# Kernel optimization log

Hardware: AMD Instinct MI355X
Metric: run time of the kernel (lower is better)

Reference implementation:

```python
import jax, jax.numpy as jnp
import numpy as np

SOS = 1

def setup_inputs() -> dict:
    key = jax.random.key(0)
    ks = jax.random.split(key, 12)
    B, S, T, H, V = 64, 128, 32, 1024, 32000
    sc = 0.02
    return {
        'encoder_outputs': jax.random.normal(ks[0], (B, S, H), jnp.float32),
        'encoder_hidden': jax.random.normal(ks[1], (1, B, H), jnp.float32),
        'target_tensor': jax.random.randint(ks[2], (B, T), 0, V),
        'embedding': jax.random.normal(ks[3], (V, H), jnp.float32) * sc,
        'Wa': jax.random.normal(ks[4], (H, H), jnp.float32) * sc,
        'ba': jnp.zeros((H,), jnp.float32),
        'Ua': jax.random.normal(ks[5], (H, H), jnp.float32) * sc,
        'bu': jnp.zeros((H,), jnp.float32),
        'Va': jax.random.normal(ks[6], (1, H), jnp.float32) * sc,
        'bv': jnp.zeros((1,), jnp.float32),
        'W_ih': jax.random.normal(ks[7], (3 * H, 2 * H), jnp.float32) * sc,
        'b_ih': jnp.zeros((3 * H,), jnp.float32),
        'W_hh': jax.random.normal(ks[8], (3 * H, H), jnp.float32) * sc,
        'b_hh': jnp.zeros((3 * H,), jnp.float32),
        'W_out': jax.random.normal(ks[9], (V, H), jnp.float32) * sc,
        'b_out': jnp.zeros((V,), jnp.float32),
    }

def reference(encoder_outputs, encoder_hidden, target_tensor, embedding,
              Wa, ba, Ua, bu, Va, bv, W_ih, b_ih, W_hh, b_hh, W_out, b_out):
    B, S, H = encoder_outputs.shape
    T = target_tensor.shape[1]
    # teacher forcing: input at step i is SOS for i=0 else target[:, i-1]
    tokens = jnp.concatenate([jnp.full((B, 1), SOS, target_tensor.dtype),
                              target_tensor[:, :-1]], axis=1)  # (B,T)
    emb = embedding[tokens]  # (B,T,H); dropout is identity (eval)
    keys_proj = jnp.einsum('bsh,gh->bsg', encoder_outputs, Ua) + bu  # Ua(keys), (B,S,H)
    h0 = encoder_hidden[0]  # (B,H)

    def step(h, x_t):
        # Bahdanau attention: Va(tanh(Wa q + Ua k))
        q = h @ Wa.T + ba  # (B,H)
        scores = jnp.einsum('bsh,h->bs', jnp.tanh(q[:, None, :] + keys_proj), Va[0]) + bv[0]
        w = jax.nn.softmax(scores, axis=-1)  # (B,S)
        ctx = jnp.einsum('bs,bsh->bh', w, encoder_outputs)
        x = jnp.concatenate([x_t, ctx], axis=-1)  # (B,2H)
        # GRU cell (PyTorch convention)
        gi = x @ W_ih.T + b_ih
        gh = h @ W_hh.T + b_hh
        ir, iz, inn = jnp.split(gi, 3, axis=-1)
        hr, hz, hn = jnp.split(gh, 3, axis=-1)
        r = jax.nn.sigmoid(ir + hr)
        z = jax.nn.sigmoid(iz + hz)
        n = jnp.tanh(inn + r * hn)
        h_new = (1.0 - z) * n + z * h
        logits = h_new @ W_out.T + b_out  # (B,V)
        return h_new, (logits, w)

    h_final, (logits, weights) = jax.lax.scan(step, h0, jnp.swapaxes(emb, 0, 1))
    log_probs = jax.nn.log_softmax(jnp.swapaxes(logits, 0, 1), axis=-1)  # (B,T,V)
    attentions = jnp.swapaxes(weights, 0, 1)  # (B,T,S)
    return log_probs, h_final[None], attentions
```

## Files before the change

kernel.cpp:

```cpp
#include <hip/hip_runtime.h>


typedef unsigned short u16;
typedef __bf16 bf16x8 __attribute__((ext_vector_type(8)));
typedef float f32x4 __attribute__((ext_vector_type(4)));
typedef u16 u16x8 __attribute__((ext_vector_type(8)));

#define DEV __device__ __forceinline__

DEV u16 f2b(float f) {
  union { float f; unsigned u; } v; v.f = f;
  unsigned r = v.u + 0x7fffu + ((v.u >> 16) & 1u);
  return (u16)(r >> 16);
}
DEV float b2f(u16 b) {
  union { unsigned u; float f; } v; v.u = ((unsigned)b) << 16;
  return v.f;
}
DEV float sigm(float x) { return 1.f / (1.f + __expf(-x)); }
DEV float ftanh(float x) {
  x = fminf(fmaxf(x, -20.f), 20.f);
  float e = __expf(2.f * x);
  return (e - 1.f) / (e + 1.f);
}
DEV void gl16(const void* g, void* l) {
  __builtin_amdgcn_global_load_lds((const __attribute__((address_space(1))) void*)g,
                                   (__attribute__((address_space(3))) void*)l, 16, 0, 0);
}

__global__ __launch_bounds__(256) void prepk(const float* __restrict__ enc, const float* __restrict__ Ua,
                                             const float* __restrict__ Wa, const float* __restrict__ Whh,
                                             const float* __restrict__ Wout, const float* __restrict__ Wih,
                                             const float* __restrict__ embd, const int* __restrict__ tgt,
                                             const float* __restrict__ eh, u16* __restrict__ enc_b,
                                             u16* __restrict__ Ua_b, u16* __restrict__ Wa_b,
                                             u16* __restrict__ Whh_b, u16* __restrict__ Wout_b,
                                             u16* __restrict__ Wih1_b, u16* __restrict__ Wih2_b,
                                             u16* __restrict__ emb_b, float* __restrict__ hf,
                                             u16* __restrict__ hb0) {
  const long q0 = 2097152;
  const long q1 = q0 + 262144;
  const long q2 = q1 + 262144;
  const long q3 = q2 + 786432;
  const long q4 = q3 + 8192000;
  const long q5 = q4 + 1572864;
  const long q6 = q5 + 524288;
  const long q7 = q6 + 16384;
  long stride = (long)gridDim.x * 256;
  for (long i = (long)blockIdx.x * 256 + threadIdx.x; i < q7; i += stride) {
    if (i < q4) {
      const float* src; u16* dst; long off;
      if (i < q0) { src = enc; dst = enc_b; off = i; }
      else if (i < q1) { src = Ua; dst = Ua_b; off = i - q0; }
      else if (i < q2) { src = Wa; dst = Wa_b; off = i - q1; }
      else if (i < q3) { src = Whh; dst = Whh_b; off = i - q2; }
      else { src = Wout; dst = Wout_b; off = i - q3; }
      float4 v = ((const float4*)src)[off];
      ushort4 o; o.x = f2b(v.x); o.y = f2b(v.y); o.z = f2b(v.z); o.w = f2b(v.w);
      ((ushort4*)dst)[off] = o;
    } else if (i < q5) {
      long off = i - q4;
      long e = off * 4;
      int row = (int)(e >> 11), col = (int)(e & 2047);
      float4 v = ((const float4*)Wih)[off];
      ushort4 o; o.x = f2b(v.x); o.y = f2b(v.y); o.z = f2b(v.z); o.w = f2b(v.w);
      u16* dst = (col < 1024) ? (Wih1_b + (size_t)row * 1024 + col)
                              : (Wih2_b + (size_t)row * 1024 + col - 1024);
      *(ushort4*)dst = o;
    } else if (i < q6) {
      long off = i - q5;
      size_t e = (size_t)off * 4;
      int h = (int)(e & 1023);
      int bt = (int)(e >> 10);
      int b = bt >> 5, t = bt & 31;
      int tok = (t == 0) ? 1 : tgt[b * 32 + t - 1];
      const float* src = embd + (size_t)tok * 1024 + h;
      float4 v = *(const float4*)src;
      ushort4 o; o.x = f2b(v.x); o.y = f2b(v.y); o.z = f2b(v.z); o.w = f2b(v.w);
      *(ushort4*)(emb_b + e) = o;
    } else {
      long off = i - q6;
      float4 v = ((const float4*)eh)[off];
      ((float4*)hf)[off] = v;
      ushort4 o; o.x = f2b(v.x); o.y = f2b(v.y); o.z = f2b(v.z); o.w = f2b(v.w);
      ((ushort4*)hb0)[off] = o;
    }
  }
}

template <int MODE>
__global__ __launch_bounds__(256) void gemm_tile(const u16* __restrict__ A, const u16* __restrict__ Bm,
                                                 const float* __restrict__ bias, float* __restrict__ Cf,
                                                 u16* __restrict__ Cb, int K, int ldc, int nTM) {
  __shared__ __attribute__((aligned(16))) u16 As[128 * 32];
  __shared__ __attribute__((aligned(16))) u16 Bs[128 * 32];
  const int tid = threadIdx.x, lane = tid & 63, w = tid >> 6;
  const int chunk = gridDim.x >> 3, wg = blockIdx.x;
  const int id = (wg & 7) * chunk + (wg >> 3);
  const int m = id % nTM, n = id / nTM;
  const int m0 = m * 128, n0 = n * 128;
  const int wm = w >> 1, wn = w & 1;
  const int l16 = lane & 15, kg = lane >> 4;
  const int srow = lane >> 2;
  const int skk = (((lane & 3) ^ ((srow >> 1) & 3)) * 8);
  const int slot = (kg ^ ((l16 >> 1) & 3)) * 8;

  f32x4 acc[4][4];
#pragma unroll
  for (int i = 0; i < 4; ++i)
#pragma unroll
    for (int j = 0; j < 4; ++j) acc[i][j] = f32x4{0.f, 0.f, 0.f, 0.f};

  for (int k0 = 0; k0 < K; k0 += 32) {
#pragma unroll
    for (int ch = 0; ch < 2; ++ch) {
      int c = w + ch * 4;
      gl16(A + (size_t)(m0 + c * 16 + srow) * K + k0 + skk, &As[c * 512]);
      gl16(Bm + (size_t)(n0 + c * 16 + srow) * K + k0 + skk, &Bs[c * 512]);
    }
    __syncthreads();
    bf16x8 av[4], bv[4];
#pragma unroll
    for (int i = 0; i < 4; ++i) av[i] = *(const bf16x8*)&As[(wm * 4 + i) * 512 + l16 * 32 + slot];
#pragma unroll
    for (int j = 0; j < 4; ++j) bv[j] = *(const bf16x8*)&Bs[(wn * 4 + j) * 512 + l16 * 32 + slot];
#pragma unroll
    for (int i = 0; i < 4; ++i)
#pragma unroll
      for (int j = 0; j < 4; ++j)
        acc[i][j] = __builtin_amdgcn_mfma_f32_16x16x32_bf16(av[i], bv[j], acc[i][j], 0, 0, 0);
    __syncthreads();
  }
#pragma unroll
  for (int i = 0; i < 4; ++i) {
    int rowb = m0 + (wm * 4 + i) * 16 + kg * 4;
#pragma unroll
    for (int j = 0; j < 4; ++j) {
      int col = n0 + (wn * 4 + j) * 16 + l16;
      float bb = (MODE == 2) ? 0.f : bias[col];
#pragma unroll
      for (int r = 0; r < 4; ++r) {
        int row = rowb + r;
        float v = acc[i][j][r] + bb;
        if (MODE == 0) Cf[(size_t)row * ldc + col] = v;
        else Cb[(size_t)row * ldc + col] = f2b(v);
      }
    }
  }
}

template <int MODE>
__global__ __launch_bounds__(256, 2) void gemm_wide(const u16* __restrict__ A, const u16* __restrict__ Bm,
                                                    const float* __restrict__ bias, float* __restrict__ Cf,
                                                    u16* __restrict__ Cb, int K, int ldc) {
  __shared__ __attribute__((aligned(16))) u16 As[128 * 32];
  __shared__ __attribute__((aligned(16))) u16 Bs[256 * 32];
  const int tid = threadIdx.x, lane = tid & 63, w = tid >> 6;
  const int chunk = gridDim.x >> 3, wg = blockIdx.x;
  const int id = (wg & 7) * chunk + (wg >> 3);
  const int r_ = id % 80;
  const int m = r_ & 15, n = 5 * (id / 80) + (r_ >> 4);
  const int m0 = m * 128, n0 = n * 256;
  const int wm = w >> 1, wn = w & 1;
  const int l16 = lane & 15, kg = lane >> 4;
  const int srow = lane >> 2;
  const int skk = (((lane & 3) ^ ((srow >> 1) & 3)) * 8);
  const int slot = (kg ^ ((l16 >> 1) & 3)) * 8;

  f32x4 acc[4][8];
#pragma unroll
  for (int i = 0; i < 4; ++i)
#pragma unroll
    for (int j = 0; j < 8; ++j) acc[i][j] = f32x4{0.f, 0.f, 0.f, 0.f};

  for (int k0 = 0; k0 < K; k0 += 32) {
#pragma unroll
    for (int ch = 0; ch < 2; ++ch) {
      int c = w + ch * 4;
      gl16(A + (size_t)(m0 + c * 16 + srow) * K + k0 + skk, &As[c * 512]);
    }
#pragma unroll
    for (int ch = 0; ch < 4; ++ch) {
      int c = w + ch * 4;
      gl16(Bm + (size_t)(n0 + c * 16 + srow) * K + k0 + skk, &Bs[c * 512]);
    }
    __syncthreads();
    bf16x8 av[4], bv[8];
#pragma unroll
    for (int i = 0; i < 4; ++i) av[i] = *(const bf16x8*)&As[(wm * 4 + i) * 512 + l16 * 32 + slot];
#pragma unroll
    for (int j = 0; j < 8; ++j) bv[j] = *(const bf16x8*)&Bs[(wn * 8 + j) * 512 + l16 * 32 + slot];
#pragma unroll
    for (int i = 0; i < 4; ++i)
#pragma unroll
      for (int j = 0; j < 8; ++j)
        acc[i][j] = __builtin_amdgcn_mfma_f32_16x16x32_bf16(av[i], bv[j], acc[i][j], 0, 0, 0);
    __syncthreads();
  }
#pragma unroll
  for (int i = 0; i < 4; ++i) {
    int rowb = m0 + (wm * 4 + i) * 16 + kg * 4;
#pragma unroll
    for (int j = 0; j < 8; ++j) {
      int col = n0 + (wn * 8 + j) * 16 + l16;
      float bb = bias[col];
#pragma unroll
      for (int r = 0; r < 4; ++r) {
        int row = rowb + r;
        float v = acc[i][j][r] + bb;
        int b_ = row & 63, t_ = row >> 6;
        size_t ro = ((size_t)b_ * 32 + t_) * ldc + col;
        if (MODE == 0) Cf[ro] = v; else Cb[ro] = f2b(v);
      }
    }
  }
}

__global__ __launch_bounds__(256) void qkghk(const u16* __restrict__ hb, const u16* __restrict__ W1,
                                             float* __restrict__ qghp) {
  const int tid = threadIdx.x, lane = tid & 63, w = tid >> 6;
  const int l16 = lane & 15, kg = lane >> 4;
  const int pg = blockIdx.x >> 2, ks = blockIdx.x & 3;
  const u16* ap = hb + (size_t)(w * 16 + l16) * 1024 + ks * 256 + kg * 8;
  const u16* bp = W1 + (size_t)(pg * 16 + l16) * 1024 + ks * 256 + kg * 8;
  f32x4 a = {0.f, 0.f, 0.f, 0.f};
#pragma unroll
  for (int k0 = 0; k0 < 256; k0 += 32)
    a = __builtin_amdgcn_mfma_f32_16x16x32_bf16(*(const bf16x8*)(ap + k0), *(const bf16x8*)(bp + k0),
                                                a, 0, 0, 0);
  const int col = pg * 16 + l16;
#pragma unroll
  for (int r = 0; r < 4; ++r) {
    int b = w * 16 + kg * 4 + r;
    qghp[(size_t)ks * 262144 + b * 4096 + col] = a[r];
  }
}

__global__ __launch_bounds__(256) void scorekq(const float* __restrict__ qghp, const float* __restrict__ ba,
                                               const float* __restrict__ Va, const u16* __restrict__ kp,
                                               float* __restrict__ sc) {
  const int b = blockIdx.x >> 3, s8 = blockIdx.x & 7;
  const int tid = threadIdx.x, lane = tid & 63, w = tid >> 6;
  __shared__ float qs[1024], vas[1024];
#pragma unroll
  for (int j = 0; j < 4; ++j) {
    int e = tid + j * 256;
    qs[e] = qghp[b * 4096 + e] + qghp[262144 + b * 4096 + e] + qghp[524288 + b * 4096 + e] +
            qghp[786432 + b * 4096 + e] + ba[e];
    vas[e] = Va[e];
  }
  __syncthreads();
#pragma unroll
  for (int si = 0; si < 4; ++si) {
    int s = s8 * 16 + w * 4 + si;
    const bf16x8* kv = (const bf16x8*)(kp + ((size_t)b * 128 + s) * 1024);
    float a = 0.f;
#pragma unroll
    for (int i2 = 0; i2 < 2; ++i2) {
      int e = lane + 64 * i2;
      bf16x8 k8 = kv[e];
#pragma unroll
      for (int j = 0; j < 8; ++j) a += vas[e * 8 + j] * ftanh(qs[e * 8 + j] + (float)k8[j]);
    }
#pragma unroll
    for (int off = 32; off; off >>= 1) a += __shfl_xor(a, off);
    if (lane == 0) sc[b * 128 + s] = a;
  }
}

__global__ __launch_bounds__(512) void wsumgate(const float* __restrict__ scb, const u16* __restrict__ encW2,
                                                const float* __restrict__ gie, const float* __restrict__ qghp,
                                                const float* __restrict__ bhh, float* __restrict__ hf,
                                                u16* __restrict__ hbW, u16* __restrict__ hall,
                                                float* __restrict__ hfin, float* __restrict__ att_out, int t) {
  const int b = blockIdx.x >> 2, cg = blockIdx.x & 3;
  const int tid = threadIdx.x, lane = tid & 63, w = tid >> 6;
  __shared__ float wsm[128];
  __shared__ float pa[3][2][256];
  if (w == 0) {
    float v0 = scb[b * 128 + lane], v1 = scb[b * 128 + 64 + lane];
    float mx = fmaxf(v0, v1);
#pragma unroll
    for (int off = 32; off; off >>= 1) mx = fmaxf(mx, __shfl_xor(mx, off));
    float e0 = __expf(v0 - mx), e1 = __expf(v1 - mx);
    float sm = e0 + e1;
#pragma unroll
    for (int off = 32; off; off >>= 1) sm += __shfl_xor(sm, off);
    float inv = 1.f / sm;
    e0 *= inv; e1 *= inv;
    wsm[lane] = e0; wsm[lane + 64] = e1;
    if (cg == 0) {
      size_t ao = ((size_t)b * 32 + t) * 128;
      att_out[ao + lane] = e0;
      att_out[ao + lane + 64] = e1;
    }
  }
  __syncthreads();
  const int ct = tid & 255, half = tid >> 8;
  const int col = cg * 256 + ct;
  float a0 = 0.f, a1 = 0.f, a2 = 0.f;
  const u16* ep = encW2 + (size_t)b * 128 * 3072 + (size_t)half * 64 * 3072 + col;
#pragma unroll 8
  for (int s = 0; s < 64; ++s) {
    float ws = wsm[half * 64 + s];
    a0 += ws * b2f(ep[0]);
    a1 += ws * b2f(ep[1024]);
    a2 += ws * b2f(ep[2048]);
    ep += 3072;
  }
  pa[0][half][ct] = a0; pa[1][half][ct] = a1; pa[2][half][ct] = a2;
  __syncthreads();
  if (tid < 256) {
    float g0 = pa[0][0][tid] + pa[0][1][tid];
    float g1 = pa[1][0][tid] + pa[1][1][tid];
    float g2 = pa[2][0][tid] + pa[2][1][tid];
    const int c2 = cg * 256 + tid;
    const float* ge = gie + ((size_t)b * 32 + t) * 3072 + c2;
    const float* qg = qghp + (size_t)b * 4096 + 1024 + c2;
    float hr = qg[0] + qg[262144] + qg[524288] + qg[786432] + bhh[c2];
    float hz = qg[1024] + qg[1024 + 262144] + qg[1024 + 524288] + qg[1024 + 786432] + bhh[c2 + 1024];
    float hn = qg[2048] + qg[2048 + 262144] + qg[2048 + 524288] + qg[2048 + 786432] + bhh[c2 + 2048];
    float rr = sigm(g0 + ge[0] + hr);
    float zz = sigm(g1 + ge[1024] + hz);
    float nn = ftanh(g2 + ge[2048] + rr * hn);
    const int i = b * 1024 + c2;
    float hp = hf[i];
    float hv = (1.f - zz) * nn + zz * hp;
    hf[i] = hv;
    u16 h16 = f2b(hv);
    hbW[i] = h16;
    hall[((size_t)t * 64 + b) * 1024 + c2] = h16;
    if (t == 31) hfin[i] = hv;
  }
}

__global__ __launch_bounds__(256) void smaxctxk(const float* __restrict__ sc, const u16* __restrict__ encb,
                                                u16* __restrict__ ctxb, float* __restrict__ att_out, int t) {
  const int b = blockIdx.x >> 2, hq = blockIdx.x & 3;
  const int tid = threadIdx.x, lane = tid & 63, w = tid >> 6;
  __shared__ float wsm[128];
  if (w == 0) {
    float v0 = sc[b * 128 + lane], v1 = sc[b * 128 + 64 + lane];
    float mx = fmaxf(v0, v1);
#pragma unroll
    for (int off = 32; off; off >>= 1) mx = fmaxf(mx, __shfl_xor(mx, off));
    float e0 = __expf(v0 - mx), e1 = __expf(v1 - mx);
    float sm = e0 + e1;
#pragma unroll
    for (int off = 32; off; off >>= 1) sm += __shfl_xor(sm, off);
    float inv = 1.f / sm;
    e0 *= inv; e1 *= inv;
    wsm[lane] = e0; wsm[lane + 64] = e1;
    if (hq == 0) {
      size_t ao = ((size_t)b * 32 + t) * 128;
      att_out[ao + lane] = e0;
      att_out[ao + lane + 64] = e1;
    }
  }
  __syncthreads();
  const int h = hq * 256 + tid;
  const u16* ep = encb + (size_t)b * 131072 + h;
  float c = 0.f;
#pragma unroll 8
  for (int s = 0; s < 128; ++s) c += wsm[s] * b2f(ep[(size_t)s * 1024]);
  ctxb[(size_t)b * 1024 + h] = f2b(c);
}

__global__ __launch_bounds__(256) void gi2w(const u16* __restrict__ ctxb, const u16* __restrict__ Wih2,
                                            float* __restrict__ gic) {
  const int tid = threadIdx.x, lane = tid & 63, w = tid >> 6;
  const int l16 = lane & 15, kg = lane >> 4;
  const int c0 = blockIdx.x * 16;
  const u16* ap = ctxb + (size_t)(w * 16 + l16) * 1024 + kg * 8;
  const u16* bp = Wih2 + (size_t)(c0 + l16) * 1024 + kg * 8;
  f32x4 a0 = {0.f, 0.f, 0.f, 0.f}, a1 = {0.f, 0.f, 0.f, 0.f};
#pragma unroll 4
  for (int k0 = 0; k0 < 1024; k0 += 64) {
    a0 = __builtin_amdgcn_mfma_f32_16x16x32_bf16(*(const bf16x8*)(ap + k0), *(const bf16x8*)(bp + k0),
                                                 a0, 0, 0, 0);
    a1 = __builtin_amdgcn_mfma_f32_16x16x32_bf16(*(const bf16x8*)(ap + k0 + 32),
                                                 *(const bf16x8*)(bp + k0 + 32), a1, 0, 0, 0);
  }
  const int col = c0 + l16;
#pragma unroll
  for (int r = 0; r < 4; ++r) {
    int b = w * 16 + kg * 4 + r;
    gic[(size_t)b * 3072 + col] = a0[r] + a1[r];
  }
}

__global__ __launch_bounds__(256) void gatesq(const float* __restrict__ gic, const float* __restrict__ gie,
                                              const float* __restrict__ qghp, const float* __restrict__ bhh,
                                              float* __restrict__ hf, u16* __restrict__ hbW,
                                              u16* __restrict__ hall, float* __restrict__ hfin, int t) {
  const int i = blockIdx.x * 256 + threadIdx.x;
  const int b = i >> 10, col = i & 1023;
  const float* gi = gic + (size_t)b * 3072 + col;
  const float* ge = gie + ((size_t)b * 32 + t) * 3072 + col;
  const float* qg = qghp + (size_t)b * 4096 + 1024 + col;
  float hr = qg[0] + qg[262144] + qg[524288] + qg[786432] + bhh[col];
  float hz = qg[1024] + qg[1024 + 262144] + qg[1024 + 524288] + qg[1024 + 786432] + bhh[col + 1024];
  float hn = qg[2048] + qg[2048 + 262144] + qg[2048 + 524288] + qg[2048 + 786432] + bhh[col + 2048];
  float rr = sigm(gi[0] + ge[0] + hr);
  float zz = sigm(gi[1024] + ge[1024] + hz);
  float nn = ftanh(gi[2048] + ge[2048] + rr * hn);
  float hp = hf[i];
  float hv = (1.f - zz) * nn + zz * hp;
  hf[i] = hv;
  u16 h16 = f2b(hv);
  hbW[i] = h16;
  hall[((size_t)t * 64 + b) * 1024 + col] = h16;
  if (t == 31) hfin[i] = hv;
}

__global__ __launch_bounds__(256) void logsoftk(const u16* __restrict__ lg, float* __restrict__ out) {
  const int row = blockIdx.x, tid = threadIdx.x, lane = tid & 63, w = tid >> 6;
  const u16x8* p = (const u16x8*)(lg + (size_t)row * 32000);
  __shared__ float red[4];
  u16x8 d[16];
#pragma unroll
  for (int j = 0; j < 16; ++j) {
    int i = tid + j * 256;
    if (i < 4000) d[j] = p[i];
  }
  float mx = -3.0e38f;
#pragma unroll
  for (int j = 0; j < 16; ++j) {
    int i = tid + j * 256;
    if (i < 4000)
#pragma unroll
      for (int k = 0; k < 8; ++k) mx = fmaxf(mx, b2f(d[j][k]));
  }
#pragma unroll
  for (int off = 32; off; off >>= 1) mx = fmaxf(mx, __shfl_xor(mx, off));
  if (lane == 0) red[w] = mx;
  __syncthreads();
  mx = fmaxf(fmaxf(red[0], red[1]), fmaxf(red[2], red[3]));
  __syncthreads();
  float s = 0.f;
#pragma unroll
  for (int j = 0; j < 16; ++j) {
    int i = tid + j * 256;
    if (i < 4000)
#pragma unroll
      for (int k = 0; k < 8; ++k) s += __expf(b2f(d[j][k]) - mx);
  }
#pragma unroll
  for (int off = 32; off; off >>= 1) s += __shfl_xor(s, off);
  if (lane == 0) red[w] = s;
  __syncthreads();
  float c = mx + __logf(red[0] + red[1] + red[2] + red[3]);
  float* op = out + (size_t)row * 32000;
#pragma unroll
  for (int j = 0; j < 16; ++j) {
    int i = tid + j * 256;
    if (i < 4000) {
      f32x4 o0, o1;
#pragma unroll
      for (int k = 0; k < 4; ++k) { o0[k] = b2f(d[j][k]) - c; o1[k] = b2f(d[j][k + 4]) - c; }
      *(f32x4*)(op + i * 8) = o0;
      *(f32x4*)(op + i * 8 + 4) = o1;
    }
  }
}

__global__ __launch_bounds__(256) void rowstatk(const float* __restrict__ lp, float* __restrict__ c) {
  int row = blockIdx.x;
  const float4* p = (const float4*)(lp + (size_t)row * 32000);
  int tid = threadIdx.x, lane = tid & 63, w = tid >> 6;
  __shared__ float redm[4], reds[4];
  float mx = -3.0e38f;
  for (int i = tid; i < 8000; i += 256) {
    float4 v = p[i];
    mx = fmaxf(mx, fmaxf(fmaxf(v.x, v.y), fmaxf(v.z, v.w)));
  }
#pragma unroll
  for (int off = 32; off; off >>= 1) mx = fmaxf(mx, __shfl_xor(mx, off));
  if (lane == 0) redm[w] = mx;
  __syncthreads();
  mx = fmaxf(fmaxf(redm[0], redm[1]), fmaxf(redm[2], redm[3]));
  float s = 0.f;
  for (int i = tid; i < 8000; i += 256) {
    float4 v = p[i];
    s += __expf(v.x - mx) + __expf(v.y - mx) + __expf(v.z - mx) + __expf(v.w - mx);
  }
#pragma unroll
  for (int off = 32; off; off >>= 1) s += __shfl_xor(s, off);
  if (lane == 0) reds[w] = s;
  __syncthreads();
  if (tid == 0) c[row] = mx + __logf(reds[0] + reds[1] + reds[2] + reds[3]);
}

__global__ __launch_bounds__(256) void subk(float* __restrict__ lp, const float* __restrict__ c) {
  const long n4 = (long)64 * 32 * 32000 / 4;
  long stride = (long)gridDim.x * 256;
  for (long i = (long)blockIdx.x * 256 + threadIdx.x; i < n4; i += stride) {
    float4 v = ((float4*)lp)[i];
    float cc = c[i / 8000];
    v.x -= cc; v.y -= cc; v.z -= cc; v.w -= cc;
    ((float4*)lp)[i] = v;
  }
}

extern "C" void kernel_launch(void* const* d_in, const int* in_sizes, int n_in, void* d_out, int out_size,
                              void* d_ws, size_t ws_size, hipStream_t stream) {
  (void)in_sizes; (void)n_in; (void)out_size;
  constexpr int B = 64, S = 128, T = 32, H = 1024, V = 32000;

  const float* enc  = (const float*)d_in[0];
  const float* ehid = (const float*)d_in[1];
  const int*   tgt  = (const int*)d_in[2];
  const float* embd = (const float*)d_in[3];
  const float* Wa   = (const float*)d_in[4];
  const float* ba   = (const float*)d_in[5];
  const float* Ua   = (const float*)d_in[6];
  const float* bu   = (const float*)d_in[7];
  const float* Va   = (const float*)d_in[8];
  const float* Wih  = (const float*)d_in[10];
  const float* bih  = (const float*)d_in[11];
  const float* Whh  = (const float*)d_in[12];
  const float* bhh  = (const float*)d_in[13];
  const float* Wout = (const float*)d_in[14];
  const float* bout = (const float*)d_in[15];

  char* wp = (char*)d_ws;
  auto alloc = [&](size_t bytes) {
    char* p = wp;
    wp += (bytes + 255) & ~(size_t)255;
    return p;
  };
  u16* enc_b  = (u16*)alloc((size_t)B * S * H * 2);
  u16* kp_b   = (u16*)alloc((size_t)B * S * H * 2);
  u16* Ua_b   = (u16*)alloc((size_t)H * H * 2);
  u16* W1_b   = (u16*)alloc((size_t)4096 * 1024 * 2);
  u16* Wih1_b = (u16*)alloc((size_t)3072 * 1024 * 2);
  u16* Wih2_b = (u16*)alloc((size_t)3072 * 1024 * 2);
  u16* Wout_b = (u16*)alloc((size_t)V * H * 2);
  u16* emb_b  = (u16*)alloc((size_t)B * T * H * 2);
  u16* hall_b = (u16*)alloc((size_t)T * B * H * 2);
  float* gie  = (float*)alloc((size_t)B * T * 3072 * 4);
  float* qghp = (float*)alloc((size_t)4 * B * 4096 * 4);
  float* scb  = (float*)alloc((size_t)B * S * 4);
  float* gic  = (float*)alloc((size_t)B * 3072 * 4);
  u16* ctx_b  = (u16*)alloc((size_t)B * H * 2);
  u16* hb0    = (u16*)alloc((size_t)B * H * 2);
  u16* hb1    = (u16*)alloc((size_t)B * H * 2);
  float* h_f  = (float*)alloc((size_t)B * H * 4);
  float* rowc = (float*)alloc(2048 * 4);
  size_t base_need = (size_t)(wp - (char*)d_ws);
  u16* encW2 = (u16*)alloc((size_t)B * S * 3072 * 2);
  bool have_w2 = ((size_t)(wp - (char*)d_ws) <= ws_size);
  u16* lg_b = (u16*)alloc((size_t)B * T * V * 2);
  bool bflog = ((size_t)(wp - (char*)d_ws) <= ws_size);
  if (base_need > ws_size) return;

  float* out_lp = (float*)d_out;
  float* out_hf = out_lp + (size_t)B * T * V;
  float* out_at = out_hf + (size_t)B * H;

  u16* Wa_slot = W1_b;
  u16* Whh_slot = W1_b + (size_t)1024 * 1024;
  prepk<<<2048, 256, 0, stream>>>(enc, Ua, Wa, Whh, Wout, Wih, embd, tgt, ehid,
                                  enc_b, Ua_b, Wa_slot, Whh_slot, Wout_b,
                                  Wih1_b, Wih2_b, emb_b, h_f, hb0);

  gemm_tile<1><<<512, 256, 0, stream>>>(enc_b, Ua_b, bu, nullptr, kp_b, H, H, 64);
  gemm_tile<0><<<384, 256, 0, stream>>>(emb_b, Wih1_b, bih, gie, nullptr, H, 3072, 16);
  if (have_w2) {
    gemm_tile<2><<<1536, 256, 0, stream>>>(enc_b, Wih2_b, nullptr, nullptr, encW2, H, 3072, 64);
  }

  for (int t = 0; t < T; ++t) {
    u16* hbR = (t & 1) ? hb1 : hb0;
    u16* hbW = (t & 1) ? hb0 : hb1;
    qkghk<<<1024, 256, 0, stream>>>(hbR, W1_b, qghp);
    scorekq<<<512, 256, 0, stream>>>(qghp, ba, Va, kp_b, scb);
    if (have_w2) {
      wsumgate<<<256, 512, 0, stream>>>(scb, encW2, gie, qghp, bhh, h_f, hbW, hall_b,
                                        out_hf, out_at, t);
    } else {
      smaxctxk<<<256, 256, 0, stream>>>(scb, enc_b, ctx_b, out_at, t);
      gi2w<<<192, 256, 0, stream>>>(ctx_b, Wih2_b, gic);
      gatesq<<<256, 256, 0, stream>>>(gic, gie, qghp, bhh, h_f, hbW, hall_b, out_hf, t);
    }
  }

  if (bflog) {
    gemm_wide<1><<<2000, 256, 0, stream>>>(hall_b, Wout_b, bout, nullptr, lg_b, H, V);
    logsoftk<<<2048, 256, 0, stream>>>(lg_b, out_lp);
  } else {
    gemm_wide<0><<<2000, 256, 0, stream>>>(hall_b, Wout_b, bout, out_lp, nullptr, H, V);
    rowstatk<<<2048, 256, 0, stream>>>(out_lp, rowc);
    subk<<<2048, 256, 0, stream>>>(out_lp, rowc);
  }
}
```

Measured before the change: 1.425 ms.

## Fuse attention scoring with weighted-sum gate kernel and transpose encW2 layout

Merges the per-step score kernel into the weighted-sum/GRU gate kernel, so each decoder step launches one fewer kernel and the scores stay in shared memory. The precomputed encoder-times-W_ih product is now produced transposed (per batch, gate column by sequence), letting each thread read contiguous 128-element vectors when forming the context-gate sums. The trade-off is a smaller grid of 128 blocks of 512 threads, so each block computes all 128 scores redundantly (twice per batch) and the GPU runs at lower parallelism.

After: 2.281 ms. +60.0%, slower.

```diff
diff --git a/kernel.cpp b/kernel.cpp
--- a/kernel.cpp
+++ b/kernel.cpp
@@ -98,7 +98,9 @@
   const int chunk = gridDim.x >> 3, wg = blockIdx.x;
   const int id = (wg & 7) * chunk + (wg >> 3);
   const int m = id % nTM, n = id / nTM;
-  const int m0 = m * 128, n0 = n * 128;
+  const int m0 = m * 128;
+  const int n0 = (MODE == 3) ? 0 : n * 128;
+  const u16* Bp = (MODE == 3) ? (Bm + (size_t)n * 131072) : Bm;
   const int wm = w >> 1, wn = w & 1;
   const int l16 = lane & 15, kg = lane >> 4;
   const int srow = lane >> 2;
@@ -116,7 +118,7 @@
     for (int ch = 0; ch < 2; ++ch) {
       int c = w + ch * 4;
       gl16(A + (size_t)(m0 + c * 16 + srow) * K + k0 + skk, &As[c * 512]);
-      gl16(Bm + (size_t)(n0 + c * 16 + srow) * K + k0 + skk, &Bs[c * 512]);
+      gl16(Bp + (size_t)(n0 + c * 16 + srow) * K + k0 + skk, &Bs[c * 512]);
     }
     __syncthreads();
     bf16x8 av[4], bv[4];
@@ -137,12 +139,13 @@
 #pragma unroll
     for (int j = 0; j < 4; ++j) {
       int col = n0 + (wn * 4 + j) * 16 + l16;
-      float bb = (MODE == 2) ? 0.f : bias[col];
+      float bb = (MODE >= 2) ? 0.f : bias[col];
 #pragma unroll
       for (int r = 0; r < 4; ++r) {
         int row = rowb + r;
         float v = acc[i][j][r] + bb;
         if (MODE == 0) Cf[(size_t)row * ldc + col] = v;
+        else if (MODE == 3) Cb[(size_t)n * 393216 + (size_t)row * 128 + col] = f2b(v);
         else Cb[(size_t)row * ldc + col] = f2b(v);
       }
     }
@@ -236,6 +239,95 @@
   }
 }
 
+__global__ __launch_bounds__(512) void attwsum(const float* __restrict__ qghp, const float* __restrict__ ba,
+                                               const float* __restrict__ Va, const u16* __restrict__ kp,
+                                               const u16* __restrict__ encW2t, const float* __restrict__ gie,
+                                               const float* __restrict__ bhh, float* __restrict__ hf,
+                                               u16* __restrict__ hbW, u16* __restrict__ hall,
+                                               float* __restrict__ hfin, float* __restrict__ att_out, int t) {
+  const int b = blockIdx.x >> 1, ch = blockIdx.x & 1;
+  const int tid = threadIdx.x, lane = tid & 63, w = tid >> 6;
+  __shared__ float qs[1024], vas[1024], wsm[128];
+#pragma unroll
+  for (int j = 0; j < 2; ++j) {
+    int e = tid + j * 512;
+    qs[e] = qghp[b * 4096 + e] + qghp[262144 + b * 4096 + e] + qghp[524288 + b * 4096 + e] +
+            qghp[786432 + b * 4096 + e] + ba[e];
+    vas[e] = Va[e];
+  }
+  __syncthreads();
+#pragma unroll 4
+  for (int si = 0; si < 16; ++si) {
+    int s = w * 16 + si;
+    const bf16x8* kv = (const bf16x8*)(kp + ((size_t)b * 128 + s) * 1024);
+    float a = 0.f;
+#pragma unroll
+    for (int i2 = 0; i2 < 2; ++i2) {
+      int e = lane + 64 * i2;
+      bf16x8 k8 = kv[e];
+#pragma unroll
+      for (int j = 0; j < 8; ++j) a += vas[e * 8 + j] * ftanh(qs[e * 8 + j] + (float)k8[j]);
+    }
+#pragma unroll
+    for (int off = 32; off; off >>= 1) a += __shfl_xor(a, off);
+    if (lane == 0) wsm[s] = a;
+  }
+  __syncthreads();
+  if (w == 0) {
+    float v0 = wsm[lane], v1 = wsm[lane + 64];
+    float mx = fmaxf(v0, v1);
+#pragma unroll
+    for (int off = 32; off; off >>= 1) mx = fmaxf(mx, __shfl_xor(mx, off));
+    float e0 = __expf(v0 - mx), e1 = __expf(v1 - mx);
+    float sm = e0 + e1;
+#pragma unroll
+    for (int off = 32; off; off >>= 1) sm += __shfl_xor(sm, off);
+    float inv = 1.f / sm;
+    e0 *= inv; e1 *= inv;
+    wsm[lane] = e0; wsm[lane + 64] = e1;
+    if (ch == 0) {
+      size_t ao = ((size_t)b * 32 + t) * 128;
+      att_out[ao + lane] = e0;
+      att_out[ao + lane + 64] = e1;
+    }
+  }
+  __syncthreads();
+  const int col = ch * 512 + tid;
+  float g0, g1, g2;
+  {
+    float ga[3];
+#pragma unroll
+    for (int gg = 0; gg < 3; ++gg) {
+      const u16x8* ep = (const u16x8*)(encW2t + (size_t)b * 393216 + (size_t)(gg * 1024 + col) * 128);
+      float a = 0.f;
+#pragma unroll
+      for (int s8 = 0; s8 < 16; ++s8) {
+        u16x8 v = ep[s8];
+#pragma unroll
+        for (int k = 0; k < 8; ++k) a += wsm[s8 * 8 + k] * b2f(v[k]);
+      }
+      ga[gg] = a;
+    }
+    g0 = ga[0]; g1 = ga[1]; g2 = ga[2];
+  }
+  const float* ge = gie + ((size_t)b * 32 + t) * 3072 + col;
+  const float* qg = qghp + (size_t)b * 4096 + 1024 + col;
+  float hr = qg[0] + qg[262144] + qg[524288] + qg[786432] + bhh[col];
+  float hz = qg[1024] + qg[1024 + 262144] + qg[1024 + 524288] + qg[1024 + 786432] + bhh[col + 1024];
+  float hn = qg[2048] + qg[2048 + 262144] + qg[2048 + 524288] + qg[2048 + 786432] + bhh[col + 2048];
+  float rr = sigm(g0 + ge[0] + hr);
+  float zz = sigm(g1 + ge[1024] + hz);
+  float nn = ftanh(g2 + ge[2048] + rr * hn);
+  const int i = b * 1024 + col;
+  float hp = hf[i];
+  float hv = (1.f - zz) * nn + zz * hp;
+  hf[i] = hv;
+  u16 h16 = f2b(hv);
+  hbW[i] = h16;
+  hall[((size_t)t * 64 + b) * 1024 + col] = h16;
+  if (t == 31) hfin[i] = hv;
+}
+
 __global__ __launch_bounds__(256) void scorekq(const float* __restrict__ qghp, const float* __restrict__ ba,
                                                const float* __restrict__ Va, const u16* __restrict__ kp,
                                                float* __restrict__ sc) {
@@ -265,72 +357,6 @@
 #pragma unroll
     for (int off = 32; off; off >>= 1) a += __shfl_xor(a, off);
     if (lane == 0) sc[b * 128 + s] = a;
-  }
-}
-
-__global__ __launch_bounds__(512) void wsumgate(const float* __restrict__ scb, const u16* __restrict__ encW2,
-                                                const float* __restrict__ gie, const float* __restrict__ qghp,
-                                                const float* __restrict__ bhh, float* __restrict__ hf,
-                                                u16* __restrict__ hbW, u16* __restrict__ hall,
-                                                float* __restrict__ hfin, float* __restrict__ att_out, int t) {
-  const int b = blockIdx.x >> 2, cg = blockIdx.x & 3;
-  const int tid = threadIdx.x, lane = tid & 63, w = tid >> 6;
-  __shared__ float wsm[128];
-  __shared__ float pa[3][2][256];
-  if (w == 0) {
-    float v0 = scb[b * 128 + lane], v1 = scb[b * 128 + 64 + lane];
-    float mx = fmaxf(v0, v1);
-#pragma unroll
-    for (int off = 32; off; off >>= 1) mx = fmaxf(mx, __shfl_xor(mx, off));
-    float e0 = __expf(v0 - mx), e1 = __expf(v1 - mx);
-    float sm = e0 + e1;
-#pragma unroll
-    for (int off = 32; off; off >>= 1) sm += __shfl_xor(sm, off);
-    float inv = 1.f / sm;
-    e0 *= inv; e1 *= inv;
-    wsm[lane] = e0; wsm[lane + 64] = e1;
-    if (cg == 0) {
-      size_t ao = ((size_t)b * 32 + t) * 128;
-      att_out[ao + lane] = e0;
-      att_out[ao + lane + 64] = e1;
-    }
-  }
-  __syncthreads();
-  const int ct = tid & 255, half = tid >> 8;
-  const int col = cg * 256 + ct;
-  float a0 = 0.f, a1 = 0.f, a2 = 0.f;
-  const u16* ep = encW2 + (size_t)b * 128 * 3072 + (size_t)half * 64 * 3072 + col;
-#pragma unroll 8
-  for (int s = 0; s < 64; ++s) {
-    float ws = wsm[half * 64 + s];
-    a0 += ws * b2f(ep[0]);
-    a1 += ws * b2f(ep[1024]);
-    a2 += ws * b2f(ep[2048]);
-    ep += 3072;
-  }
-  pa[0][half][ct] = a0; pa[1][half][ct] = a1; pa[2][half][ct] = a2;
-  __syncthreads();
-  if (tid < 256) {
-    float g0 = pa[0][0][tid] + pa[0][1][tid];
-    float g1 = pa[1][0][tid] + pa[1][1][tid];
-    float g2 = pa[2][0][tid] + pa[2][1][tid];
-    const int c2 = cg * 256 + tid;
-    const float* ge = gie + ((size_t)b * 32 + t) * 3072 + c2;
-    const float* qg = qghp + (size_t)b * 4096 + 1024 + c2;
-    float hr = qg[0] + qg[262144] + qg[524288] + qg[786432] + bhh[c2];
-    float hz = qg[1024] + qg[1024 + 262144] + qg[1024 + 524288] + qg[1024 + 786432] + bhh[c2 + 1024];
-    float hn = qg[2048] + qg[2048 + 262144] + qg[2048 + 524288] + qg[2048 + 786432] + bhh[c2 + 2048];
-    float rr = sigm(g0 + ge[0] + hr);
-    float zz = sigm(g1 + ge[1024] + hz);
-    float nn = ftanh(g2 + ge[2048] + rr * hn);
-    const int i = b * 1024 + c2;
-    float hp = hf[i];
-    float hv = (1.f - zz) * nn + zz * hp;
-    hf[i] = hv;
-    u16 h16 = f2b(hv);
-    hbW[i] = h16;
-    hall[((size_t)t * 64 + b) * 1024 + c2] = h16;
-    if (t == 31) hfin[i] = hv;
   }
 }
 
@@ -548,7 +574,7 @@
   float* h_f  = (float*)alloc((size_t)B * H * 4);
   float* rowc = (float*)alloc(2048 * 4);
   size_t base_need = (size_t)(wp - (char*)d_ws);
-  u16* encW2 = (u16*)alloc((size_t)B * S * 3072 * 2);
+  u16* encW2t = (u16*)alloc((size_t)B * 3072 * S * 2);
   bool have_w2 = ((size_t)(wp - (char*)d_ws) <= ws_size);
   u16* lg_b = (u16*)alloc((size_t)B * T * V * 2);
   bool bflog = ((size_t)(wp - (char*)d_ws) <= ws_size);
@@ -567,18 +593,18 @@
   gemm_tile<1><<<512, 256, 0, stream>>>(enc_b, Ua_b, bu, nullptr, kp_b, H, H, 64);
   gemm_tile<0><<<384, 256, 0, stream>>>(emb_b, Wih1_b, bih, gie, nullptr, H, 3072, 16);
   if (have_w2) {
-    gemm_tile<2><<<1536, 256, 0, stream>>>(enc_b, Wih2_b, nullptr, nullptr, encW2, H, 3072, 64);
+    gemm_tile<3><<<1536, 256, 0, stream>>>(Wih2_b, enc_b, nullptr, nullptr, encW2t, H, 0, 24);
   }
 
   for (int t = 0; t < T; ++t) {
     u16* hbR = (t & 1) ? hb1 : hb0;
     u16* hbW = (t & 1) ? hb0 : hb1;
     qkghk<<<1024, 256, 0, stream>>>(hbR, W1_b, qghp);
-    scorekq<<<512, 256, 0, stream>>>(qghp, ba, Va, kp_b, scb);
     if (have_w2) {
-      wsumgate<<<256, 512, 0, stream>>>(scb, encW2, gie, qghp, bhh, h_f, hbW, hall_b,
-                                        out_hf, out_at, t);
+      attwsum<<<128, 512, 0, stream>>>(qghp, ba, Va, kp_b, encW2t, gie, bhh, h_f, hbW, hall_b,
+                                       out_hf, out_at, t);
     } else {
+      scorekq<<<512, 256, 0, stream>>>(qghp, ba, Va, kp_b, scb);
       smaxctxk<<<256, 256, 0, stream>>>(scb, enc_b, ctx_b, out_at, t);
       gi2w<<<192, 256, 0, stream>>>(ctx_b, Wih2_b, gic);
       gatesq<<<256, 256, 0, stream>>>(gic, gie, qghp, bhh, h_f, hbW, hall_b, out_hf, t);
```
